# Performance work log

Hardware: AMD Instinct MI355X
Metric: run time of the kernel (lower is better)

## Reference

```python
import jax, jax.numpy as jnp
import numpy as np

B, N, K = 2, 8192, 16
D_IN, D_OUT = 8, 64
EPS = 1e-5  # BatchNorm eps (torch default)


def setup_inputs() -> dict:
    key = jax.random.key(0)
    ks = jax.random.split(key, 4)
    return {
        "xyz": jax.random.normal(ks[0], (B, N, 3), jnp.float32),
        "features": jax.random.normal(ks[1], (B, N, D_IN), jnp.float32),
        # Conv2d(10, d_out, 1, bias=False) weight -> [d_out, 10]
        "W1": jax.random.normal(ks[2], (D_OUT, 10), jnp.float32) * 0.1,
        "gamma1": jnp.ones((D_OUT,), jnp.float32),
        "beta1": jnp.zeros((D_OUT,), jnp.float32),
        # Conv2d(d_out, d_out, 1, bias=False) weight -> [d_out, d_out]
        "W2": jax.random.normal(ks[3], (D_OUT, D_OUT), jnp.float32) * 0.1,
        "gamma2": jnp.ones((D_OUT,), jnp.float32),
        "beta2": jnp.zeros((D_OUT,), jnp.float32),
    }


def _bn_relu(x, gamma, beta):
    # BatchNorm2d in training mode: batch stats over (B, N, K) per channel (last axis here)
    mean = jnp.mean(x, axis=(0, 1, 2))
    var = jnp.var(x, axis=(0, 1, 2))
    return jax.nn.relu((x - mean) * jax.lax.rsqrt(var + EPS) * gamma + beta)


def reference(xyz, features, W1, gamma1, beta1, W2, gamma2, beta2):
    # knn_point: k nearest neighbors under squared euclidean distance (self included)
    sq = jnp.sum(xyz * xyz, axis=-1)                                   # [B,N]
    d = sq[:, :, None] + sq[:, None, :] - 2.0 * jnp.einsum("bnc,bmc->bnm", xyz, xyz)
    _, knn_idx = jax.lax.top_k(-d, K)                                  # [B,N,K]

    # index_points: per-batch gather of neighbor coordinates
    neighbor_xyz = jax.vmap(lambda pts, idx: pts[idx])(xyz, knn_idx)   # [B,N,K,3]
    # (original also gathers neighbor_features but never uses them -> dead code)

    center = xyz[:, :, None, :]                                        # [B,N,1,3]
    relative_xyz = neighbor_xyz - center                               # [B,N,K,3]
    dist = jnp.sum(relative_xyz * relative_xyz, axis=-1, keepdims=True)
    spatial_feat = jnp.concatenate(
        [jnp.broadcast_to(center, neighbor_xyz.shape), neighbor_xyz, relative_xyz, dist],
        axis=-1,
    )                                                                  # [B,N,K,10]

    # 1x1 conv MLP (channels-last einsum == Conv2d kernel_size=1)
    h = _bn_relu(jnp.einsum("bnkc,dc->bnkd", spatial_feat, W1), gamma1, beta1)
    h = _bn_relu(jnp.einsum("bnkc,dc->bnkd", h, W2), gamma2, beta2)
    return jnp.transpose(h, (0, 3, 1, 2))                              # [B,D_OUT,N,K]
```

## Files before the change

kernel.cpp:

```cpp
#include <hip/hip_runtime.h>
#include <hip/hip_bf16.h>
#include <math.h>

#define NB 2
#define NPTS 8192
#define KNN 16
#define DOUT 64
#define NKROWS (NPTS*KNN)
#define TOTROWS (NB*NPTS*KNN)
#define EPSV 1e-5

__device__ __forceinline__ float mulrn(float a, float b) { float t = a*b; asm("" : "+v"(t)); return t; }
__device__ __forceinline__ float addrn(float a, float b) { float t = a+b; asm("" : "+v"(t)); return t; }

__device__ __forceinline__ float sq_np(float x, float y, float z) {
  return __builtin_fmaf(z, z, __builtin_fmaf(y, y, mulrn(x, x)));
}
__device__ __forceinline__ float dist_np(float qx, float qy, float qz, float qsq,
                                         float cx, float cy, float cz, float csq) {
  const float dot = __builtin_fmaf(qz, cz, __builtin_fmaf(qy, cy, mulrn(qx, cx)));
  return addrn(__builtin_fmaf(-2.0f, dot, qsq), csq);
}

__device__ __forceinline__ float dpp_down1_f(float x) {
  return __int_as_float(__builtin_amdgcn_update_dpp(0, __float_as_int(x), 0x101, 0xF, 0xF, true));
}
__device__ __forceinline__ int dpp_down1_i(int x) {
  return __builtin_amdgcn_update_dpp(0, x, 0x101, 0xF, 0xF, true);
}

__global__ __launch_bounds__(512, 8) void knn_kernel(const float* __restrict__ xyz,
                                                     int* __restrict__ knn) {
  __shared__ float4 sc[2048];
  const int tid = threadIdx.x;
  const int wv = tid >> 6, lane = tid & 63;
  const int q = blockIdx.x * 8 + wv;
  const int b = q >> 13, qi = q & (NPTS - 1);
  const float* xb = xyz + (size_t)b * NPTS * 3;
  const float qx = xb[qi*3+0], qy = xb[qi*3+1], qz = xb[qi*3+2];
  const float qsq = sq_np(qx, qy, qz);

  float D = __builtin_inff();
  int   I = 0;
  float w = __builtin_inff();
  const bool is15 = (lane == 15);

  for (int tl = 0; tl < 4; ++tl) {
    if (tl) __syncthreads();
    for (int i = tid; i < 2048; i += 512) {
      const int j = tl*2048 + i;
      const float x = xb[j*3+0], y = xb[j*3+1], z = xb[j*3+2];
      sc[i] = make_float4(x, y, z, sq_np(x, y, z));
    }
    __syncthreads();
    for (int it = 0; it < 32; ++it) {
      const float4 c = sc[it*64 + lane];
      const float d = dist_np(qx, qy, qz, qsq, c.x, c.y, c.z, c.w);
      const int jb = tl*2048 + it*64;
      unsigned long long m = __ballot(d < w);
      while (m) {
        const int src = (int)__builtin_ctzll(m);
        m &= (m - 1ull);
        const float dc = __int_as_float(__builtin_amdgcn_readlane(__float_as_int(d), src));
        const int   ic = jb + src;
        float Dn = dpp_down1_f(D);
        int   In = dpp_down1_i(I);
        Dn = is15 ? -__builtin_inff() : Dn;
        const bool up   = dc < Dn;
        const bool here = dc < D;
        D = up ? Dn : (here ? dc : D);
        I = up ? In : (here ? ic : I);
      }
      w = __int_as_float(__builtin_amdgcn_readlane(__float_as_int(D), 0));
    }
  }
  if (lane < 16) knn[(size_t)q*KNN + (15 - lane)] = I;
}

__global__ __launch_bounds__(256) void stats1_kernel(const float* __restrict__ xyz,
                                                     const int* __restrict__ knn,
                                                     float* __restrict__ part1) {
  float acc[65];
#pragma unroll
  for (int i = 0; i < 65; ++i) acc[i] = 0.f;
  const int t0 = blockIdx.x * 256 + threadIdx.x;
  for (int itr = 0; itr < 4; ++itr) {
    const int r = t0 + itr * 65536;
    const int q = r >> 4;
    const int b = q >> 13, qi = q & (NPTS - 1);
    const float* xb = xyz + (size_t)b * NPTS * 3;
    const int j = knn[r];
    const float cx = xb[qi*3], cy = xb[qi*3+1], cz = xb[qi*3+2];
    const float nx = xb[(size_t)j*3], ny = xb[(size_t)j*3+1], nz = xb[(size_t)j*3+2];
    const float rx = nx-cx, ry = ny-cy, rz = nz-cz;
    const float dist = rx*rx + ry*ry + rz*rz;
    const float sf[10] = {cx,cy,cz,nx,ny,nz,rx,ry,rz,dist};
#pragma unroll
    for (int a = 0; a < 10; ++a) acc[a] += sf[a];
    int idx = 10;
#pragma unroll
    for (int a = 0; a < 10; ++a) {
#pragma unroll
      for (int bb = a; bb < 10; ++bb) { acc[idx] += sf[a]*sf[bb]; ++idx; }
    }
  }
  __shared__ float red[4][65];
  const int lane = threadIdx.x & 63, wv = threadIdx.x >> 6;
#pragma unroll
  for (int i = 0; i < 65; ++i) {
    float v = acc[i];
    for (int off = 1; off < 64; off <<= 1) v += __shfl_xor(v, off);
    if (lane == 0) red[wv][i] = v;
  }
  __syncthreads();
  if (threadIdx.x < 65) {
    part1[blockIdx.x*65 + threadIdx.x] =
      red[0][threadIdx.x] + red[1][threadIdx.x] + red[2][threadIdx.x] + red[3][threadIdx.x];
  }
}

__global__ __launch_bounds__(128) void reduce1_kernel(const float* __restrict__ part1,
                                                      const float* __restrict__ W1,
                                                      const float* __restrict__ g1,
                                                      const float* __restrict__ b1,
                                                      float* __restrict__ sb1) {
  __shared__ double tot[65];
  const int t = threadIdx.x;
  if (t < 65) {
    double s = 0.0;
    for (int p = 0; p < 256; ++p) s += (double)part1[p*65 + t];
    tot[t] = s;
  }
  __syncthreads();
  if (t < 64) {
    const double R = (double)TOTROWS;
    double wrow[10];
    for (int j = 0; j < 10; ++j) wrow[j] = (double)W1[t*10 + j];
    double mean = 0.0;
    for (int j = 0; j < 10; ++j) mean += tot[j] * wrow[j];
    mean /= R;
    double msq = 0.0;
    int idx = 10;
    for (int a = 0; a < 10; ++a)
      for (int bb = a; bb < 10; ++bb) {
        const double f = (a == bb) ? 1.0 : 2.0;
        msq += f * wrow[a] * wrow[bb] * tot[idx]; ++idx;
      }
    msq /= R;
    const double var = msq - mean*mean;
    const double inv = 1.0 / sqrt(var + EPSV);
    const double sc = (double)g1[t] * inv;
    sb1[t]      = (float)sc;
    sb1[64 + t] = (float)((double)b1[t] - mean*sc);
  }
}

__global__ __launch_bounds__(256) void main_kernel(const float* __restrict__ xyz,
                                                   const int* __restrict__ knn,
                                                   const float* __restrict__ W1,
                                                   const float* __restrict__ W2,
                                                   const float* __restrict__ sb1,
                                                   float* __restrict__ out,
                                                   float* __restrict__ part2) {
  __shared__ float red[4][128];
  const int tid = threadIdx.x;
  const int r = blockIdx.x*256 + tid;
  const int q = r >> 4;
  const int b = q >> 13, qi = q & (NPTS - 1);
  const float* xb = xyz + (size_t)b * NPTS * 3;
  const int j = knn[r];
  const float cx = xb[qi*3], cy = xb[qi*3+1], cz = xb[qi*3+2];
  const float nx = xb[(size_t)j*3], ny = xb[(size_t)j*3+1], nz = xb[(size_t)j*3+2];
  const float rx = nx-cx, ry = ny-cy, rz = nz-cz;
  const float dist = rx*rx + ry*ry + rz*rz;
  const float sf[10] = {cx,cy,cz,nx,ny,nz,rx,ry,rz,dist};
  float h1[64];
#pragma unroll
  for (int c = 0; c < 64; ++c) {
    float a = 0.f;
#pragma unroll
    for (int jj = 0; jj < 10; ++jj) a += sf[jj] * W1[c*10 + jj];
    h1[c] = fmaxf(fmaf(a, sb1[c], sb1[64 + c]), 0.f);
  }
  const int lane = tid & 63, wv = tid >> 6;
  const int rb = r & (NKROWS - 1);
  float* outb = out + (size_t)b * DOUT * NKROWS;
#pragma unroll 1
  for (int c = 0; c < 64; ++c) {
    float a = 0.f;
#pragma unroll
    for (int jj = 0; jj < 64; ++jj) a += h1[jj] * W2[c*64 + jj];
    outb[(size_t)c * NKROWS + rb] = a;
    float s = a, s2 = a*a;
    for (int off = 1; off < 64; off <<= 1) { s += __shfl_xor(s, off); s2 += __shfl_xor(s2, off); }
    if (lane == 0) { red[wv][c] = s; red[wv][64 + c] = s2; }
  }
  __syncthreads();
  if (tid < 128) {
    part2[blockIdx.x*128 + tid] = red[0][tid] + red[1][tid] + red[2][tid] + red[3][tid];
  }
}

__global__ __launch_bounds__(1024) void reduce2_kernel(const float* __restrict__ part2,
                                                       const float* __restrict__ g2,
                                                       const float* __restrict__ b2,
                                                       float* __restrict__ sb2) {
  __shared__ double stage[8][128];
  __shared__ double tot[128];
  const int t = threadIdx.x;
  const int c = t & 127, chunk = t >> 7;
  double s = 0.0;
  for (int p = chunk*128; p < chunk*128 + 128; ++p) s += (double)part2[p*128 + c];
  stage[chunk][c] = s;
  __syncthreads();
  if (t < 128) {
    double v = 0.0;
    for (int k = 0; k < 8; ++k) v += stage[k][t];
    tot[t] = v;
  }
  __syncthreads();
  if (t < 64) {
    const double R = (double)TOTROWS;
    const double mean = tot[t] / R;
    const double var = tot[64 + t] / R - mean*mean;
    const double inv = 1.0 / sqrt(var + EPSV);
    const double sc = (double)g2[t] * inv;
    sb2[t]      = (float)sc;
    sb2[64 + t] = (float)((double)b2[t] - mean*sc);
  }
}

__global__ __launch_bounds__(256) void bn2_kernel(float* __restrict__ out,
                                                  const float* __restrict__ sb2) {
  const int n4 = TOTROWS * DOUT / 4;
  float4* o4 = (float4*)out;
  for (int i = blockIdx.x*256 + threadIdx.x; i < n4; i += gridDim.x * 256) {
    const int c = (i >> 15) & 63;
    const float sc = sb2[c], bi = sb2[64 + c];
    float4 v = o4[i];
    v.x = fmaxf(fmaf(v.x, sc, bi), 0.f);
    v.y = fmaxf(fmaf(v.y, sc, bi), 0.f);
    v.z = fmaxf(fmaf(v.z, sc, bi), 0.f);
    v.w = fmaxf(fmaf(v.w, sc, bi), 0.f);
    o4[i] = v;
  }
}

extern "C" void kernel_launch(void* const* d_in, const int* in_sizes, int n_in,
                              void* d_out, int out_size, void* d_ws, size_t ws_size,
                              hipStream_t stream) {
  (void)in_sizes; (void)n_in; (void)out_size; (void)ws_size;
  const float* xyz = (const float*)d_in[0];
  const float* W1 = (const float*)d_in[2];
  const float* g1 = (const float*)d_in[3];
  const float* b1 = (const float*)d_in[4];
  const float* W2 = (const float*)d_in[5];
  const float* g2 = (const float*)d_in[6];
  const float* b2 = (const float*)d_in[7];
  float* out = (float*)d_out;

  char* ws = (char*)d_ws;
  int*   knn   = (int*)ws;
  float* part1 = (float*)(ws + 1048576);
  float* part2 = (float*)(ws + 1048576 + 66560);
  float* sb1   = (float*)(ws + 1048576 + 66560 + 524288);
  float* sb2   = sb1 + 128;

  hipLaunchKernelGGL(knn_kernel,    dim3(2048), dim3(512),  0, stream, xyz, knn);
  hipLaunchKernelGGL(stats1_kernel, dim3(256),  dim3(256),  0, stream, xyz, knn, part1);
  hipLaunchKernelGGL(reduce1_kernel,dim3(1),    dim3(128),  0, stream, part1, W1, g1, b1, sb1);
  hipLaunchKernelGGL(main_kernel,   dim3(1024), dim3(256),  0, stream, xyz, knn, W1, W2, sb1, out, part2);
  hipLaunchKernelGGL(reduce2_kernel,dim3(1),    dim3(1024), 0, stream, part2, g2, b2, sb2);
  hipLaunchKernelGGL(bn2_kernel,    dim3(2048), dim3(256),  0, stream, out, sb2);
}
```

Measured before the change: 220.7 us.

## Recompute MLP in final pass instead of storing and re-reading pre-BN output

After: 284.2 us. 1.29x slower.

```diff
diff --git a/kernel.cpp b/kernel.cpp
--- a/kernel.cpp
+++ b/kernel.cpp
@@ -155,16 +155,11 @@
   }
 }
 
-__global__ __launch_bounds__(256) void main_kernel(const float* __restrict__ xyz,
-                                                   const int* __restrict__ knn,
-                                                   const float* __restrict__ W1,
-                                                   const float* __restrict__ W2,
-                                                   const float* __restrict__ sb1,
-                                                   float* __restrict__ out,
-                                                   float* __restrict__ part2) {
-  __shared__ float red[4][128];
-  const int tid = threadIdx.x;
-  const int r = blockIdx.x*256 + tid;
+__device__ __forceinline__ void compute_h1(const float* __restrict__ xyz,
+                                           const int* __restrict__ knn,
+                                           const float* __restrict__ W1,
+                                           const float* __restrict__ sb1,
+                                           int r, float* h1) {
   const int q = r >> 4;
   const int b = q >> 13, qi = q & (NPTS - 1);
   const float* xb = xyz + (size_t)b * NPTS * 3;
@@ -174,7 +169,6 @@
   const float rx = nx-cx, ry = ny-cy, rz = nz-cz;
   const float dist = rx*rx + ry*ry + rz*rz;
   const float sf[10] = {cx,cy,cz,nx,ny,nz,rx,ry,rz,dist};
-  float h1[64];
 #pragma unroll
   for (int c = 0; c < 64; ++c) {
     float a = 0.f;
@@ -182,15 +176,25 @@
     for (int jj = 0; jj < 10; ++jj) a += sf[jj] * W1[c*10 + jj];
     h1[c] = fmaxf(fmaf(a, sb1[c], sb1[64 + c]), 0.f);
   }
+}
+
+__global__ __launch_bounds__(256) void stats2_kernel(const float* __restrict__ xyz,
+                                                     const int* __restrict__ knn,
+                                                     const float* __restrict__ W1,
+                                                     const float* __restrict__ W2,
+                                                     const float* __restrict__ sb1,
+                                                     float* __restrict__ part2) {
+  __shared__ float red[4][128];
+  const int tid = threadIdx.x;
+  const int r = blockIdx.x*256 + tid;
+  float h1[64];
+  compute_h1(xyz, knn, W1, sb1, r, h1);
   const int lane = tid & 63, wv = tid >> 6;
-  const int rb = r & (NKROWS - 1);
-  float* outb = out + (size_t)b * DOUT * NKROWS;
 #pragma unroll 1
   for (int c = 0; c < 64; ++c) {
     float a = 0.f;
 #pragma unroll
     for (int jj = 0; jj < 64; ++jj) a += h1[jj] * W2[c*64 + jj];
-    outb[(size_t)c * NKROWS + rb] = a;
     float s = a, s2 = a*a;
     for (int off = 1; off < 64; off <<= 1) { s += __shfl_xor(s, off); s2 += __shfl_xor(s2, off); }
     if (lane == 0) { red[wv][c] = s; red[wv][64 + c] = s2; }
@@ -230,19 +234,26 @@
   }
 }
 
-__global__ __launch_bounds__(256) void bn2_kernel(float* __restrict__ out,
-                                                  const float* __restrict__ sb2) {
-  const int n4 = TOTROWS * DOUT / 4;
-  float4* o4 = (float4*)out;
-  for (int i = blockIdx.x*256 + threadIdx.x; i < n4; i += gridDim.x * 256) {
-    const int c = (i >> 15) & 63;
-    const float sc = sb2[c], bi = sb2[64 + c];
-    float4 v = o4[i];
-    v.x = fmaxf(fmaf(v.x, sc, bi), 0.f);
-    v.y = fmaxf(fmaf(v.y, sc, bi), 0.f);
-    v.z = fmaxf(fmaf(v.z, sc, bi), 0.f);
-    v.w = fmaxf(fmaf(v.w, sc, bi), 0.f);
-    o4[i] = v;
+__global__ __launch_bounds__(256) void final_kernel(const float* __restrict__ xyz,
+                                                    const int* __restrict__ knn,
+                                                    const float* __restrict__ W1,
+                                                    const float* __restrict__ W2,
+                                                    const float* __restrict__ sb1,
+                                                    const float* __restrict__ sb2,
+                                                    float* __restrict__ out) {
+  const int tid = threadIdx.x;
+  const int r = blockIdx.x*256 + tid;
+  float h1[64];
+  compute_h1(xyz, knn, W1, sb1, r, h1);
+  const int b = r >> 17;
+  const int rb = r & (NKROWS - 1);
+  float* outb = out + (size_t)b * DOUT * NKROWS;
+#pragma unroll 1
+  for (int c = 0; c < 64; ++c) {
+    float a = 0.f;
+#pragma unroll
+    for (int jj = 0; jj < 64; ++jj) a += h1[jj] * W2[c*64 + jj];
+    outb[(size_t)c * NKROWS + rb] = fmaxf(fmaf(a, sb2[c], sb2[64 + c]), 0.f);
   }
 }
 
@@ -269,7 +280,7 @@
   hipLaunchKernelGGL(knn_kernel,    dim3(2048), dim3(512),  0, stream, xyz, knn);
   hipLaunchKernelGGL(stats1_kernel, dim3(256),  dim3(256),  0, stream, xyz, knn, part1);
   hipLaunchKernelGGL(reduce1_kernel,dim3(1),    dim3(128),  0, stream, part1, W1, g1, b1, sb1);
-  hipLaunchKernelGGL(main_kernel,   dim3(1024), dim3(256),  0, stream, xyz, knn, W1, W2, sb1, out, part2);
+  hipLaunchKernelGGL(stats2_kernel, dim3(1024), dim3(256),  0, stream, xyz, knn, W1, W2, sb1, part2);
   hipLaunchKernelGGL(reduce2_kernel,dim3(1),    dim3(1024), 0, stream, part2, g2, b2, sb2);
-  hipLaunchKernelGGL(bn2_kernel,    dim3(2048), dim3(256),  0, stream, out, sb2);
-}
+  hipLaunchKernelGGL(final_kernel,  dim3(1024), dim3(256),  0, stream, xyz, knn, W1, W2, sb1, sb2, out);
+}
```
